# Performance work log

Hardware: AMD Instinct MI355X
Metric: run time of the kernel (lower is better)

## Reference

```python
import jax, jax.numpy as jnp
import numpy as np

B, S, H, NH, HD = 2, 2048, 4096, 32, 128
THETA = 10000.0


def rotate_half(x):
    x1, x2 = jnp.split(x, 2, axis=-1)
    return jnp.concatenate((-x2, x1), axis=-1)


def setup_inputs() -> dict:
    key = jax.random.key(0)
    ks = jax.random.split(key, 6)
    hidden_states = jax.random.normal(ks[0], (B, S, H), dtype=jnp.float32)
    # additive causal mask, [1,1,S,S]
    causal = jnp.triu(jnp.full((S, S), -1e9, dtype=jnp.float32), k=1)
    attention_mask = causal[None, None, :, :]
    scale = 0.02
    Wq = jax.random.normal(ks[1], (H, H), dtype=jnp.float32) * scale
    Wk = jax.random.normal(ks[2], (H, H), dtype=jnp.float32) * scale
    Wv = jax.random.normal(ks[3], (H, H), dtype=jnp.float32) * scale
    Wo = jax.random.normal(ks[4], (H, H), dtype=jnp.float32) * scale
    return {"hidden_states": hidden_states, "attention_mask": attention_mask,
            "Wq": Wq, "Wk": Wk, "Wv": Wv, "Wo": Wo}


def _rope_tables(seq_len, dtype):
    inv_freq = 1.0 / (THETA ** (jnp.arange(0, HD, 2, dtype=jnp.float32) / HD))
    t = jnp.arange(seq_len, dtype=jnp.float32)
    freqs = jnp.einsum('i,j->ij', t, inv_freq)          # [S, HD/2]
    emb = jnp.concatenate((freqs, freqs), axis=-1)       # [S, HD]
    return jnp.cos(emb).astype(dtype), jnp.sin(emb).astype(dtype)


def reference(hidden_states, attention_mask, Wq, Wk, Wv, Wo):
    b, s, _ = hidden_states.shape
    # nn.Linear: y = x @ W.T
    q = jnp.einsum('bsh,oh->bso', hidden_states, Wq).reshape(b, s, NH, HD).transpose(0, 2, 1, 3)
    k = jnp.einsum('bsh,oh->bso', hidden_states, Wk).reshape(b, s, NH, HD).transpose(0, 2, 1, 3)
    v = jnp.einsum('bsh,oh->bso', hidden_states, Wv).reshape(b, s, NH, HD).transpose(0, 2, 1, 3)
    cos, sin = _rope_tables(s, q.dtype)                  # [S, HD] broadcast over b,h
    q = q * cos + rotate_half(q) * sin
    k = k * cos + rotate_half(k) * sin
    scores = jnp.einsum('bhqd,bhkd->bhqk', q, k) / jnp.sqrt(jnp.asarray(HD, q.dtype))
    scores = scores + attention_mask
    attn = jax.nn.softmax(scores.astype(jnp.float32), axis=-1).astype(q.dtype)
    out = jnp.einsum('bhqk,bhkd->bhqd', attn, v)
    out = out.transpose(0, 2, 1, 3).reshape(b, s, H)
    return jnp.einsum('bsh,oh->bso', out, Wo)
```

## Files before the change

### kernel.cpp

```cpp
#include <hip/hip_runtime.h>
#include <stdint.h>

typedef __attribute__((ext_vector_type(4))) float f32x4;
typedef __attribute__((ext_vector_type(8))) short bf16x8;
typedef __attribute__((ext_vector_type(4))) unsigned int u32x4;

__device__ __forceinline__ short f2bf(float x) {
  unsigned int u = __builtin_bit_cast(unsigned int, x);
  unsigned int r = (u + 0x7fffu + ((u >> 16) & 1u)) >> 16;
  return (short)r;
}
__device__ __forceinline__ float bf2f(short s) {
  unsigned int u = ((unsigned int)(unsigned short)s) << 16;
  return __builtin_bit_cast(float, u);
}
__device__ __forceinline__ unsigned pkbf(float lo, float hi) {
  unsigned r;
  asm("v_cvt_pk_bf16_f32 %0, %1, %2" : "=v"(r) : "v"(lo), "v"(hi));
  return r;
}

__device__ __forceinline__ void gload_lds16(const void* g, void* l) {
  __builtin_amdgcn_global_load_lds(
      (const __attribute__((address_space(1))) void*)g,
      (__attribute__((address_space(3))) void*)l, 16, 0, 0);
}

__global__ __launch_bounds__(256) void cvt4(const float* __restrict__ a,
                                            const float* __restrict__ b,
                                            const float* __restrict__ c,
                                            const float* __restrict__ d,
                                            short* __restrict__ oa,
                                            short* __restrict__ ob,
                                            short* __restrict__ oc,
                                            short* __restrict__ od, int n) {
  const float* in = (blockIdx.y == 0) ? a : (blockIdx.y == 1) ? b : (blockIdx.y == 2) ? c : d;
  short* out = (blockIdx.y == 0) ? oa : (blockIdx.y == 1) ? ob : (blockIdx.y == 2) ? oc : od;
  int idx = blockIdx.x * blockDim.x + threadIdx.x;
  int stride = gridDim.x * blockDim.x;
  for (int i = idx * 4; i < n; i += stride * 4) {
    float4 v = *(const float4*)(in + i);
    short4 o;
    o.x = f2bf(v.x); o.y = f2bf(v.y); o.z = f2bf(v.z); o.w = f2bf(v.w);
    *(short4*)(out + i) = o;
  }
}

__global__ __launch_bounds__(256) void cvt_bf16(const float* __restrict__ in,
                                                short* __restrict__ out, int n) {
  int idx = blockIdx.x * blockDim.x + threadIdx.x;
  int stride = gridDim.x * blockDim.x;
  for (int i = idx * 4; i < n; i += stride * 4) {
    float4 v = *(const float4*)(in + i);
    short4 o;
    o.x = f2bf(v.x); o.y = f2bf(v.y); o.z = f2bf(v.z); o.w = f2bf(v.w);
    *(short4*)(out + i) = o;
  }
}

__global__ __launch_bounds__(256) void rope_table_k(float2* __restrict__ tab) {
  int idx = blockIdx.x * 256 + threadIdx.x;
  int s = idx >> 6, j = idx & 63;
  float invf = powf(10000.0f, -((float)j) / 64.0f);
  float a = (float)s * invf;
  tab[idx] = make_float2(cosf(a), sinf(a));
}

__global__ __launch_bounds__(256) void rope_apply_k(short* __restrict__ Qb,
                                                    short* __restrict__ Kb,
                                                    const float2* __restrict__ tab) {
  bool isK = (blockIdx.y != 0);
  short* base = isK ? Kb : Qb;
  float post = isK ? 1.0f : (0.08838834764831845f * 1.4426950408889634f);
  int token = blockIdx.x;
  int s = token & 2047;
  short* rowp = base + (size_t)token * 4096;
  const float2* trow = tab + s * 64;
  for (int u = threadIdx.x; u < 512; u += 256) {
    int h = u >> 4;
    int d0 = (u & 15) * 4;
    short* p1 = rowp + h * 128 + d0;
    short* p2 = p1 + 64;
    short4 a = *(short4*)p1, b = *(short4*)p2;
    short4 ra, rb;
#pragma unroll
    for (int j = 0; j < 4; ++j) {
      short aj = (&a.x)[j], bj = (&b.x)[j];
      float qa = bf2f(aj), qb = bf2f(bj);
      float2 cs = trow[d0 + j];
      (&ra.x)[j] = f2bf((qa * cs.x - qb * cs.y) * post);
      (&rb.x)[j] = f2bf((qb * cs.x + qa * cs.y) * post);
    }
    *(short4*)p1 = ra;
    *(short4*)p2 = rb;
  }
}

template <int MODE>
__global__ __launch_bounds__(512) void gemm256(const short* __restrict__ A,
                                               const short* __restrict__ Bw,
                                               void* __restrict__ out) {
  __shared__ __attribute__((aligned(16))) short smem[3 * 16384];
  int wg = blockIdx.x;
  int xcd = wg & 7, i = wg >> 3;
  int by = xcd * 2 + (i >> 4);
  int bx = i & 15;
  int tid = threadIdx.x;
  int w = tid >> 6, lane = tid & 63;
  int l16 = lane & 15, l4 = lane >> 4;
  int wm = w >> 2, wn = w & 3;

  f32x4 acc[8][4] = {};

  const short* Ab = A + (size_t)(by * 256) * 4096;
  const short* Bb = Bw + (size_t)(bx * 256) * 4096;
  int idx0 = tid, idx1 = 512 + tid;
  int r0 = idx0 >> 2, c0l = (idx0 & 3) ^ (r0 & 3);
  int r1 = idx1 >> 2, c1l = (idx1 & 3) ^ (r1 & 3);
  int db0 = (0 * 512 + w * 64) * 8;
  int db1 = (1 * 512 + w * 64) * 8;

  auto STAGE = [&](int kt, int ob) {
    gload_lds16(Ab + (size_t)r0 * 4096 + kt * 32 + c0l * 8, &smem[ob + db0]);
    gload_lds16(Ab + (size_t)r1 * 4096 + kt * 32 + c1l * 8, &smem[ob + db1]);
    gload_lds16(Bb + (size_t)r0 * 4096 + kt * 32 + c0l * 8, &smem[ob + 8192 + db0]);
    gload_lds16(Bb + (size_t)r1 * 4096 + kt * 32 + c1l * 8, &smem[ob + 8192 + db1]);
  };

  int o0 = 0, o1 = 16384, o2 = 32768;
  STAGE(0, o0);
  STAGE(1, o1);

  const int physc = l4 ^ (l16 & 3);
  const int arow = wm * 128 + l16;
  const int brow = wn * 64 + l16;

  auto COMPUTE = [&](int ob) {
    const short* lA = &smem[ob];
    const short* lB = &smem[ob + 8192];
    bf16x8 af[4], bfr[4];
#pragma unroll
    for (int nf = 0; nf < 4; ++nf)
      bfr[nf] = *(const bf16x8*)&lB[(brow + nf * 16) * 32 + physc * 8];
#pragma unroll
    for (int mf = 0; mf < 4; ++mf)
      af[mf] = *(const bf16x8*)&lA[(arow + mf * 16) * 32 + physc * 8];
    __builtin_amdgcn_s_setprio(1);
#pragma unroll
    for (int mf = 0; mf < 4; ++mf)
#pragma unroll
      for (int nf = 0; nf < 4; ++nf)
        acc[mf][nf] = __builtin_amdgcn_mfma_f32_16x16x32_bf16(af[mf], bfr[nf], acc[mf][nf], 0, 0, 0);
    __builtin_amdgcn_s_setprio(0);
#pragma unroll
    for (int mf = 0; mf < 4; ++mf)
      af[mf] = *(const bf16x8*)&lA[(arow + 64 + mf * 16) * 32 + physc * 8];
    __builtin_amdgcn_s_setprio(1);
#pragma unroll
    for (int mf = 0; mf < 4; ++mf)
#pragma unroll
      for (int nf = 0; nf < 4; ++nf)
        acc[mf + 4][nf] = __builtin_amdgcn_mfma_f32_16x16x32_bf16(af[mf], bfr[nf], acc[mf + 4][nf], 0, 0, 0);
    __builtin_amdgcn_s_setprio(0);
  };

  for (int t = 0; t < 127; ++t) {
    asm volatile("s_waitcnt vmcnt(4)" ::: "memory");
    __builtin_amdgcn_s_barrier();
    asm volatile("" ::: "memory");
    if (t + 2 < 128) STAGE(t + 2, o2);
    COMPUTE(o0);
    int tmp = o0; o0 = o1; o1 = o2; o2 = tmp;
  }
  asm volatile("s_waitcnt vmcnt(0)" ::: "memory");
  __builtin_amdgcn_s_barrier();
  asm volatile("" ::: "memory");
  COMPUTE(o0);

  int orow0 = by * 256 + wm * 128;
  int ocol0 = bx * 256 + wn * 64;
#pragma unroll
  for (int mf = 0; mf < 8; ++mf)
#pragma unroll
    for (int nf = 0; nf < 4; ++nf)
#pragma unroll
      for (int ii = 0; ii < 4; ++ii) {
        int r = orow0 + mf * 16 + l4 * 4 + ii;
        int c = ocol0 + nf * 16 + l16;
        float v = acc[mf][nf][ii];
        if constexpr (MODE == 0) {
          ((short*)out)[(size_t)r * 4096 + c] = f2bf(v);
        } else if constexpr (MODE == 1) {
          ((float*)out)[(size_t)r * 4096 + c] = v;
        } else {
          int bb = r >> 11, ss = r & 2047;
          int h = c >> 7, d = c & 127;
          ((short*)out)[(((size_t)((bb * 32 + h) * 128 + d)) << 11) + ss] = f2bf(v);
        }
      }
}

__global__ __launch_bounds__(256, 3) void attn_k(const short* __restrict__ Qb,
                                                 const short* __restrict__ Kb,
                                                 const short* __restrict__ Vt,
                                                 short* __restrict__ AO) {
  __shared__ __attribute__((aligned(16))) short smem[2 * 8192];
  int p = blockIdx.x;
  int bh = p & 63;
  int qt = 15 - (p >> 6);
  int b = bh >> 5, h = bh & 31;
  int tid = threadIdx.x, w = tid >> 6, lane = tid & 63;
  int l16 = lane & 15, l4 = lane >> 4;

  const int nt = 2 * qt + 2;
  const int qbase = qt * 128 + w * 32;

  bf16x8 qf[2][4];
  {
    const short* Qg = Qb + (size_t)(b * 2048 + qbase + l16) * 4096 + h * 128 + l4 * 8;
#pragma unroll
    for (int mg = 0; mg < 2; ++mg)
#pragma unroll
      for (int kk = 0; kk < 4; ++kk)
        qf[mg][kk] = *(const bf16x8*)(Qg + (size_t)mg * 16 * 4096 + kk * 32);
  }

  f32x4 oacc[2][8] = {};
  float mrun[2] = {-1e30f, -1e30f}, lsum[2] = {0.f, 0.f};

  const short* Kbase = Kb + (size_t)(b * 2048) * 4096 + h * 128;
  const short* Vbase = Vt + (size_t)bh * 128 * 2048;

  const int srowK = l4, skbK = l16;

  auto STAGE = [&](int t, int sel) {
    short* lK = &smem[sel * 8192];
#pragma unroll
    for (int ii = 0; ii < 4; ++ii) {
      int s = w * 4 + ii;
      int rowK = s * 4 + srowK;
      int srcK = skbK ^ (rowK & 15);
      gload_lds16(Kbase + (size_t)(t * 64 + rowK) * 4096 + srcK * 8, &lK[s * 512]);
    }
  };

  STAGE(0, 0);
  __syncthreads();

  const int src0 = l16 | ((2 * (l4 & 1)) << 4);
  const int src1 = src0 | 16;
  const bool hiA = (l4 >> 1) != 0;

  for (int t = 0; t < nt; ++t) {
    int sel = t & 1;
    if (t + 1 < nt) STAGE(t + 1, sel ^ 1);
    const short* lK = &smem[sel * 8192];

    bool skip = (t * 64 > qbase + 31);
    if (!skip) {
      f32x4 sacc[2][4] = {};
#pragma unroll
      for (int kk = 0; kk < 4; ++kk) {
#pragma unroll
        for (int n4 = 0; n4 < 4; ++n4) {
          int row = n4 * 16 + l16;
          int phys = (kk * 4 + l4) ^ (row & 15);
          bf16x8 kf = *(const bf16x8*)&lK[row * 128 + phys * 8];
          sacc[0][n4] = __builtin_amdgcn_mfma_f32_16x16x32_bf16(kf, qf[0][kk], sacc[0][n4], 0, 0, 0);
          sacc[1][n4] = __builtin_amdgcn_mfma_f32_16x16x32_bf16(kf, qf[1][kk], sacc[1][n4], 0, 0, 0);
        }
      }

      if (t * 64 + 63 > qbase) {
#pragma unroll
        for (int mg = 0; mg < 2; ++mg) {
          int q = qbase + mg * 16 + l16;
#pragma unroll
          for (int n4 = 0; n4 < 4; ++n4)
#pragma unroll
            for (int i = 0; i < 4; ++i) {
              int kv = t * 64 + n4 * 16 + l4 * 4 + i;
              if (kv > q) sacc[mg][n4][i] = -1e30f;
            }
        }
      }

#pragma unroll
      for (int mg = 0; mg < 2; ++mg) {
        float v0 = fmaxf(fmaxf(sacc[mg][0][0], sacc[mg][0][1]), fmaxf(sacc[mg][0][2], sacc[mg][0][3]));
        float v1 = fmaxf(fmaxf(sacc[mg][1][0], sacc[mg][1][1]), fmaxf(sacc[mg][1][2], sacc[mg][1][3]));
        float v2 = fmaxf(fmaxf(sacc[mg][2][0], sacc[mg][2][1]), fmaxf(sacc[mg][2][2], sacc[mg][2][3]));
        float v3 = fmaxf(fmaxf(sacc[mg][3][0], sacc[mg][3][1]), fmaxf(sacc[mg][3][2], sacc[mg][3][3]));
        float vm = fmaxf(fmaxf(v0, v1), fmaxf(v2, v3));
        vm = fmaxf(vm, __shfl_xor(vm, 16));
        vm = fmaxf(vm, __shfl_xor(vm, 32));
        float mn = mrun[mg];
        if (!__all(vm - mn <= 8.0f)) {
          float mnew = fmaxf(mn, vm);
          float fsc = __builtin_amdgcn_exp2f(mn - mnew);
          mrun[mg] = mnew;
          lsum[mg] *= fsc;
#pragma unroll
          for (int dg = 0; dg < 8; ++dg) oacc[mg][dg] *= fsc;
          mn = mnew;
        }
        float psum = 0.f;
#pragma unroll
        for (int n4 = 0; n4 < 4; ++n4)
#pragma unroll
          for (int i = 0; i < 4; ++i) {
            float e = __builtin_amdgcn_exp2f(sacc[mg][n4][i] - mn);
            sacc[mg][n4][i] = e;
            psum += e;
          }
        psum += __shfl_xor(psum, 16);
        psum += __shfl_xor(psum, 32);
        lsum[mg] += psum;
      }

      bf16x8 pb[2][2];
#pragma unroll
      for (int mg = 0; mg < 2; ++mg)
#pragma unroll
        for (int c = 0; c < 2; ++c) {
          unsigned pk0h0 = pkbf(sacc[mg][2 * c][0], sacc[mg][2 * c][1]);
          unsigned pk0h1 = pkbf(sacc[mg][2 * c][2], sacc[mg][2 * c][3]);
          unsigned pk1h0 = pkbf(sacc[mg][2 * c + 1][0], sacc[mg][2 * c + 1][1]);
          unsigned pk1h1 = pkbf(sacc[mg][2 * c + 1][2], sacc[mg][2 * c + 1][3]);
          unsigned s00 = __shfl((int)pk0h0, src0), s10 = __shfl((int)pk1h0, src0);
          unsigned s01 = __shfl((int)pk0h1, src0), s11 = __shfl((int)pk1h1, src0);
          unsigned t00 = __shfl((int)pk0h0, src1), t10 = __shfl((int)pk1h0, src1);
          unsigned t01 = __shfl((int)pk0h1, src1), t11 = __shfl((int)pk1h1, src1);
          u32x4 uw;
          uw[0] = hiA ? s10 : s00;
          uw[1] = hiA ? s11 : s01;
          uw[2] = hiA ? t10 : t00;
          uw[3] = hiA ? t11 : t01;
          pb[mg][c] = __builtin_bit_cast(bf16x8, uw);
        }

#pragma unroll
      for (int c = 0; c < 2; ++c) {
        const short* Vg = Vbase + t * 64 + c * 32 + l4 * 8;
#pragma unroll
        for (int dg = 0; dg < 8; ++dg) {
          bf16x8 vf = *(const bf16x8*)(Vg + (size_t)(dg * 16 + l16) * 2048);
          oacc[0][dg] = __builtin_amdgcn_mfma_f32_16x16x32_bf16(vf, pb[0][c], oacc[0][dg], 0, 0, 0);
          oacc[1][dg] = __builtin_amdgcn_mfma_f32_16x16x32_bf16(vf, pb[1][c], oacc[1][dg], 0, 0, 0);
        }
      }
    }
    __syncthreads();
  }

  short* reg = &smem[w * 4096];
  float rls0 = 1.0f / lsum[0], rls1 = 1.0f / lsum[1];
#pragma unroll
  for (int mg = 0; mg < 2; ++mg) {
    float rls = mg ? rls1 : rls0;
    int qloc = mg * 16 + l16;
#pragma unroll
    for (int dg = 0; dg < 8; ++dg) {
      unsigned u0 = pkbf(oacc[mg][dg][0] * rls, oacc[mg][dg][1] * rls);
      unsigned u1 = pkbf(oacc[mg][dg][2] * rls, oacc[mg][dg][3] * rls);
      int c16 = dg * 2 + (l4 >> 1);
      int phys = c16 ^ (qloc & 7);
      int sidx = qloc * 128 + phys * 8 + (l4 & 1) * 4;
      *(uint2*)&reg[sidx] = make_uint2(u0, u1);
    }
  }
#pragma unroll
  for (int pass = 0; pass < 8; ++pass) {
    int qloc = pass * 4 + l4;
    int phys = l16 ^ (qloc & 7);
    bf16x8 v = *(const bf16x8*)&reg[qloc * 128 + phys * 8];
    int qg = qt * 128 + w * 32 + qloc;
    *(bf16x8*)(AO + (size_t)(b * 2048 + qg) * 4096 + h * 128 + l16 * 8) = v;
  }
}

extern "C" void kernel_launch(void* const* d_in, const int* in_sizes, int n_in,
                              void* d_out, int out_size, void* d_ws, size_t ws_size,
                              hipStream_t stream) {
  const float* X = (const float*)d_in[0];
  const float* Wq = (const float*)d_in[2];
  const float* Wk = (const float*)d_in[3];
  const float* Wv = (const float*)d_in[4];
  const float* Wo = (const float*)d_in[5];

  char* ws = (char*)d_ws;
  const size_t SEG = 32ull << 20;
  short* Xb  = (short*)(ws + 0 * SEG);
  short* Wqb = (short*)(ws + 1 * SEG);
  short* Wkb = (short*)(ws + 2 * SEG);
  short* Wvb = (short*)(ws + 3 * SEG);
  short* Qb  = (short*)(ws + 4 * SEG);
  short* Kb  = (short*)(ws + 5 * SEG);
  float2* tab = (float2*)(ws + 6 * SEG);

  const int NE = 4096 * 4096;
  cvt4<<<dim3(2048, 4), 256, 0, stream>>>(X, Wq, Wk, Wv, Xb, Wqb, Wkb, Wvb, NE);
  rope_table_k<<<512, 256, 0, stream>>>(tab);

  gemm256<0><<<256, 512, 0, stream>>>(Xb, Wqb, Qb);
  gemm256<0><<<256, 512, 0, stream>>>(Xb, Wkb, Kb);
  short* Vtb = Wqb;
  gemm256<2><<<256, 512, 0, stream>>>(Xb, Wvb, Vtb);

  rope_apply_k<<<dim3(4096, 2), 256, 0, stream>>>(Qb, Kb, tab);

  short* AO = Xb;
  attn_k<<<1024, 256, 0, stream>>>(Qb, Kb, Vtb, AO);

  short* Wob = Wkb;
  cvt_bf16<<<2048, 256, 0, stream>>>(Wo, Wob, NE);
  gemm256<1><<<256, 512, 0, stream>>>(AO, Wob, (float*)d_out);
}
```

Measured before the change: 843.1 us.

## Stage V tiles through swizzled LDS and deepen K prefetch to two tiles

The attention kernel now loads V tiles asynchronously into a swizzled LDS buffer instead of reading them directly from global memory for each MFMA. K prefetch is deepened to two tiles ahead, with manual vmcnt waits and split barriers so V for the next tile loads while the current tile's QK and softmax run. This targets global-load latency on the PV matmul. In exchange, LDS use grows from 32 KB to 48 KB per block, which may cut occupancy, and the tile loop now carries extra barriers and hand-counted waits.

```diff
diff --git a/kernel.cpp b/kernel.cpp
--- a/kernel.cpp
+++ b/kernel.cpp
@@ -204,7 +204,7 @@
                                                  const short* __restrict__ Kb,
                                                  const short* __restrict__ Vt,
                                                  short* __restrict__ AO) {
-  __shared__ __attribute__((aligned(16))) short smem[2 * 8192];
+  __shared__ __attribute__((aligned(16))) short smem[24576];
   int p = blockIdx.x;
   int bh = p & 63;
   int qt = 15 - (p >> 6);
@@ -232,8 +232,9 @@
   const short* Vbase = Vt + (size_t)bh * 128 * 2048;
 
   const int srowK = l4, skbK = l16;
-
-  auto STAGE = [&](int t, int sel) {
+  const int srowV = lane >> 3, skbV = lane & 7;
+
+  auto STAGE_K = [&](int t, int sel) {
     short* lK = &smem[sel * 8192];
 #pragma unroll
     for (int ii = 0; ii < 4; ++ii) {
@@ -243,22 +244,35 @@
       gload_lds16(Kbase + (size_t)(t * 64 + rowK) * 4096 + srcK * 8, &lK[s * 512]);
     }
   };
-
-  STAGE(0, 0);
-  __syncthreads();
+  auto STAGE_V = [&](int t) {
+    short* lV = &smem[16384];
+#pragma unroll
+    for (int ii = 0; ii < 4; ++ii) {
+      int s = w * 4 + ii;
+      int rowV = s * 8 + srowV;
+      int srcV = skbV ^ (rowV & 7);
+      gload_lds16(Vbase + (size_t)rowV * 2048 + t * 64 + srcV * 8, &lV[s * 512]);
+    }
+  };
+
+  STAGE_V(0);
+  STAGE_K(0, 0);
+  STAGE_K(1, 1);
+  asm volatile("s_waitcnt vmcnt(4)" ::: "memory");
+  __builtin_amdgcn_s_barrier();
+  asm volatile("" ::: "memory");
 
   const int src0 = l16 | ((2 * (l4 & 1)) << 4);
   const int src1 = src0 | 16;
   const bool hiA = (l4 >> 1) != 0;
 
   for (int t = 0; t < nt; ++t) {
-    int sel = t & 1;
-    if (t + 1 < nt) STAGE(t + 1, sel ^ 1);
-    const short* lK = &smem[sel * 8192];
-
+    const short* lK = &smem[(t & 1) * 8192];
+    const short* lV = &smem[16384];
     bool skip = (t * 64 > qbase + 31);
+
+    f32x4 sacc[2][4] = {};
     if (!skip) {
-      f32x4 sacc[2][4] = {};
 #pragma unroll
       for (int kk = 0; kk < 4; ++kk) {
 #pragma unroll
@@ -317,7 +331,16 @@
         psum += __shfl_xor(psum, 32);
         lsum[mg] += psum;
       }
-
+    }
+
+    if (t == nt - 1)
+      asm volatile("s_waitcnt vmcnt(0)" ::: "memory");
+    else
+      asm volatile("s_waitcnt vmcnt(4)" ::: "memory");
+    __builtin_amdgcn_s_barrier();
+    asm volatile("" ::: "memory");
+
+    if (!skip) {
       bf16x8 pb[2][2];
 #pragma unroll
       for (int mg = 0; mg < 2; ++mg)
@@ -340,17 +363,27 @@
         }
 
 #pragma unroll
-      for (int c = 0; c < 2; ++c) {
-        const short* Vg = Vbase + t * 64 + c * 32 + l4 * 8;
+      for (int c = 0; c < 2; ++c)
 #pragma unroll
         for (int dg = 0; dg < 8; ++dg) {
-          bf16x8 vf = *(const bf16x8*)(Vg + (size_t)(dg * 16 + l16) * 2048);
+          int d = dg * 16 + l16;
+          int phys = (c * 4 + l4) ^ (d & 7);
+          bf16x8 vf = *(const bf16x8*)&lV[d * 64 + phys * 8];
           oacc[0][dg] = __builtin_amdgcn_mfma_f32_16x16x32_bf16(vf, pb[0][c], oacc[0][dg], 0, 0, 0);
           oacc[1][dg] = __builtin_amdgcn_mfma_f32_16x16x32_bf16(vf, pb[1][c], oacc[1][dg], 0, 0, 0);
         }
-      }
-    }
-    __syncthreads();
+    }
+
+    __builtin_amdgcn_s_barrier();
+    asm volatile("" ::: "memory");
+    if (t + 1 < nt) STAGE_V(t + 1);
+    if (t + 2 < nt) STAGE_K(t + 2, t & 1);
+    if (t + 2 < nt)
+      asm volatile("s_waitcnt vmcnt(8)" ::: "memory");
+    else if (t + 1 < nt)
+      asm volatile("s_waitcnt vmcnt(4)" ::: "memory");
+    __builtin_amdgcn_s_barrier();
+    asm volatile("" ::: "memory");
   }
 
   short* reg = &smem[w * 4096];
```

After: 761.6 us. -9.7%, faster.

## Restructure GEMM into 8-phase double-buffered K=64 pipeline and stage V via LDS

Applied to the files above, without the earlier changes.

The GEMM moves from a 3-stage K=32 ring buffer to a double-buffered K=64 tile with eight compute phases per two tiles. A and B loads are interleaved between phases, with a barrier after each phase, so global-to-LDS traffic overlaps MFMA work. Separately, the attention kernel now stages V tiles into LDS with an XOR swizzle alongside K, instead of reading V straight from global memory per MFMA. This doubles attention LDS use and drops the occupancy hint of 3, which may lower occupancy. The many per-phase barriers add synchronisation overhead.

```diff
diff --git a/kernel.cpp b/kernel.cpp
--- a/kernel.cpp
+++ b/kernel.cpp
@@ -97,14 +97,14 @@
 }
 
 template <int MODE>
-__global__ __launch_bounds__(512) void gemm256(const short* __restrict__ A,
-                                               const short* __restrict__ Bw,
-                                               void* __restrict__ out) {
-  __shared__ __attribute__((aligned(16))) short smem[3 * 16384];
+__global__ __launch_bounds__(512) void gemm8p(const short* __restrict__ A,
+                                              const short* __restrict__ Bw,
+                                              void* __restrict__ out) {
+  __shared__ __attribute__((aligned(16))) short smem[2 * 32768];
   int wg = blockIdx.x;
-  int xcd = wg & 7, i = wg >> 3;
-  int by = xcd * 2 + (i >> 4);
-  int bx = i & 15;
+  int xcd = wg & 7, ii = wg >> 3;
+  int by = xcd * 2 + (ii >> 4);
+  int bx = ii & 15;
   int tid = threadIdx.x;
   int w = tid >> 6, lane = tid & 63;
   int l16 = lane & 15, l4 = lane >> 4;
@@ -114,68 +114,83 @@
 
   const short* Ab = A + (size_t)(by * 256) * 4096;
   const short* Bb = Bw + (size_t)(bx * 256) * 4096;
-  int idx0 = tid, idx1 = 512 + tid;
-  int r0 = idx0 >> 2, c0l = (idx0 & 3) ^ (r0 & 3);
-  int r1 = idx1 >> 2, c1l = (idx1 & 3) ^ (r1 & 3);
-  int db0 = (0 * 512 + w * 64) * 8;
-  int db1 = (1 * 512 + w * 64) * 8;
-
-  auto STAGE = [&](int kt, int ob) {
-    gload_lds16(Ab + (size_t)r0 * 4096 + kt * 32 + c0l * 8, &smem[ob + db0]);
-    gload_lds16(Ab + (size_t)r1 * 4096 + kt * 32 + c1l * 8, &smem[ob + db1]);
-    gload_lds16(Bb + (size_t)r0 * 4096 + kt * 32 + c0l * 8, &smem[ob + 8192 + db0]);
-    gload_lds16(Bb + (size_t)r1 * 4096 + kt * 32 + c1l * 8, &smem[ob + 8192 + db1]);
+
+  auto STAGE_MAT = [&](int kt, int isB) {
+    const short* src = isB ? Bb : Ab;
+    int ob = (kt & 1) * 32768 + isB * 16384;
+#pragma unroll
+    for (int j = 0; j < 4; ++j) {
+      int c = j * 512 + tid;
+      int row = c >> 3;
+      int sc = (c & 7) ^ (row & 7);
+      gload_lds16(src + (size_t)row * 4096 + kt * 64 + sc * 8, &smem[ob + c * 8]);
+    }
   };
 
-  int o0 = 0, o1 = 16384, o2 = 32768;
-  STAGE(0, o0);
-  STAGE(1, o1);
-
-  const int physc = l4 ^ (l16 & 3);
-  const int arow = wm * 128 + l16;
-  const int brow = wn * 64 + l16;
-
-  auto COMPUTE = [&](int ob) {
+  bf16x8 bfr[4];
+  auto PHASE = [&](int ob, int kk, int mh, bool loadB) {
     const short* lA = &smem[ob];
-    const short* lB = &smem[ob + 8192];
-    bf16x8 af[4], bfr[4];
-#pragma unroll
-    for (int nf = 0; nf < 4; ++nf)
-      bfr[nf] = *(const bf16x8*)&lB[(brow + nf * 16) * 32 + physc * 8];
+    const short* lB = &smem[ob + 16384];
+    if (loadB) {
+#pragma unroll
+      for (int nf = 0; nf < 4; ++nf) {
+        int row = wn * 64 + nf * 16 + l16;
+        int phys = (kk * 4 + l4) ^ (row & 7);
+        bfr[nf] = *(const bf16x8*)&lB[row * 64 + phys * 8];
+      }
+    }
+    bf16x8 af[4];
+#pragma unroll
+    for (int mf = 0; mf < 4; ++mf) {
+      int row = wm * 128 + mh * 64 + mf * 16 + l16;
+      int phys = (kk * 4 + l4) ^ (row & 7);
+      af[mf] = *(const bf16x8*)&lA[row * 64 + phys * 8];
+    }
+    __builtin_amdgcn_s_setprio(1);
 #pragma unroll
     for (int mf = 0; mf < 4; ++mf)
-      af[mf] = *(const bf16x8*)&lA[(arow + mf * 16) * 32 + physc * 8];
-    __builtin_amdgcn_s_setprio(1);
-#pragma unroll
-    for (int mf = 0; mf < 4; ++mf)
 #pragma unroll
       for (int nf = 0; nf < 4; ++nf)
-        acc[mf][nf] = __builtin_amdgcn_mfma_f32_16x16x32_bf16(af[mf], bfr[nf], acc[mf][nf], 0, 0, 0);
+        acc[mh * 4 + mf][nf] =
+            __builtin_amdgcn_mfma_f32_16x16x32_bf16(af[mf], bfr[nf], acc[mh * 4 + mf][nf], 0, 0, 0);
     __builtin_amdgcn_s_setprio(0);
-#pragma unroll
-    for (int mf = 0; mf < 4; ++mf)
-      af[mf] = *(const bf16x8*)&lA[(arow + 64 + mf * 16) * 32 + physc * 8];
-    __builtin_amdgcn_s_setprio(1);
-#pragma unroll
-    for (int mf = 0; mf < 4; ++mf)
-#pragma unroll
-      for (int nf = 0; nf < 4; ++nf)
-        acc[mf + 4][nf] = __builtin_amdgcn_mfma_f32_16x16x32_bf16(af[mf], bfr[nf], acc[mf + 4][nf], 0, 0, 0);
-    __builtin_amdgcn_s_setprio(0);
+    __builtin_amdgcn_s_barrier();
+    asm volatile("" ::: "memory");
   };
 
-  for (int t = 0; t < 127; ++t) {
+  STAGE_MAT(0, 0);
+  STAGE_MAT(0, 1);
+  asm volatile("s_waitcnt vmcnt(0)" ::: "memory");
+  __builtin_amdgcn_s_barrier();
+  asm volatile("" ::: "memory");
+
+  const int b0 = 0, b1 = 32768;
+  for (int i = 0; i < 32; ++i) {
+    int kt1 = 2 * i + 1;
+
+    STAGE_MAT(kt1, 0);
     asm volatile("s_waitcnt vmcnt(4)" ::: "memory");
     __builtin_amdgcn_s_barrier();
     asm volatile("" ::: "memory");
-    if (t + 2 < 128) STAGE(t + 2, o2);
-    COMPUTE(o0);
-    int tmp = o0; o0 = o1; o1 = o2; o2 = tmp;
-  }
-  asm volatile("s_waitcnt vmcnt(0)" ::: "memory");
-  __builtin_amdgcn_s_barrier();
-  asm volatile("" ::: "memory");
-  COMPUTE(o0);
+    PHASE(b0, 0, 0, true);
+    STAGE_MAT(kt1, 1);
+    PHASE(b0, 0, 1, false);
+    PHASE(b0, 1, 0, true);
+    PHASE(b0, 1, 1, false);
+    if (i + 1 < 32) {
+      STAGE_MAT(2 * i + 2, 0);
+      asm volatile("s_waitcnt vmcnt(4)" ::: "memory");
+    } else {
+      asm volatile("s_waitcnt vmcnt(0)" ::: "memory");
+    }
+    __builtin_amdgcn_s_barrier();
+    asm volatile("" ::: "memory");
+    PHASE(b1, 0, 0, true);
+    if (i + 1 < 32) STAGE_MAT(2 * i + 2, 1);
+    PHASE(b1, 0, 1, false);
+    PHASE(b1, 1, 0, true);
+    PHASE(b1, 1, 1, false);
+  }
 
   int orow0 = by * 256 + wm * 128;
   int ocol0 = bx * 256 + wn * 64;
@@ -184,10 +199,10 @@
 #pragma unroll
     for (int nf = 0; nf < 4; ++nf)
 #pragma unroll
-      for (int ii = 0; ii < 4; ++ii) {
-        int r = orow0 + mf * 16 + l4 * 4 + ii;
+      for (int k = 0; k < 4; ++k) {
+        int r = orow0 + mf * 16 + l4 * 4 + k;
         int c = ocol0 + nf * 16 + l16;
-        float v = acc[mf][nf][ii];
+        float v = acc[mf][nf][k];
         if constexpr (MODE == 0) {
           ((short*)out)[(size_t)r * 4096 + c] = f2bf(v);
         } else if constexpr (MODE == 1) {
@@ -200,11 +215,11 @@
       }
 }
 
-__global__ __launch_bounds__(256, 3) void attn_k(const short* __restrict__ Qb,
-                                                 const short* __restrict__ Kb,
-                                                 const short* __restrict__ Vt,
-                                                 short* __restrict__ AO) {
-  __shared__ __attribute__((aligned(16))) short smem[2 * 8192];
+__global__ __launch_bounds__(256) void attn_k(const short* __restrict__ Qb,
+                                              const short* __restrict__ Kb,
+                                              const short* __restrict__ Vt,
+                                              short* __restrict__ AO) {
+  __shared__ __attribute__((aligned(16))) short smem[2 * 16384];
   int p = blockIdx.x;
   int bh = p & 63;
   int qt = 15 - (p >> 6);
@@ -232,15 +247,20 @@
   const short* Vbase = Vt + (size_t)bh * 128 * 2048;
 
   const int srowK = l4, skbK = l16;
+  const int srowV = lane >> 3, skbV = lane & 7;
 
   auto STAGE = [&](int t, int sel) {
-    short* lK = &smem[sel * 8192];
+    short* lK = &smem[sel * 16384];
+    short* lV = lK + 8192;
 #pragma unroll
     for (int ii = 0; ii < 4; ++ii) {
       int s = w * 4 + ii;
       int rowK = s * 4 + srowK;
       int srcK = skbK ^ (rowK & 15);
       gload_lds16(Kbase + (size_t)(t * 64 + rowK) * 4096 + srcK * 8, &lK[s * 512]);
+      int rowV = s * 8 + srowV;
+      int srcV = skbV ^ (rowV & 7);
+      gload_lds16(Vbase + (size_t)rowV * 2048 + t * 64 + srcV * 8, &lV[s * 512]);
     }
   };
 
@@ -254,7 +274,8 @@
   for (int t = 0; t < nt; ++t) {
     int sel = t & 1;
     if (t + 1 < nt) STAGE(t + 1, sel ^ 1);
-    const short* lK = &smem[sel * 8192];
+    const short* lK = &smem[sel * 16384];
+    const short* lV = lK + 8192;
 
     bool skip = (t * 64 > qbase + 31);
     if (!skip) {
@@ -340,15 +361,15 @@
         }
 
 #pragma unroll
-      for (int c = 0; c < 2; ++c) {
-        const short* Vg = Vbase + t * 64 + c * 32 + l4 * 8;
+      for (int c = 0; c < 2; ++c)
 #pragma unroll
         for (int dg = 0; dg < 8; ++dg) {
-          bf16x8 vf = *(const bf16x8*)(Vg + (size_t)(dg * 16 + l16) * 2048);
+          int d = dg * 16 + l16;
+          int phys = (c * 4 + l4) ^ (d & 7);
+          bf16x8 vf = *(const bf16x8*)&lV[d * 64 + phys * 8];
           oacc[0][dg] = __builtin_amdgcn_mfma_f32_16x16x32_bf16(vf, pb[0][c], oacc[0][dg], 0, 0, 0);
           oacc[1][dg] = __builtin_amdgcn_mfma_f32_16x16x32_bf16(vf, pb[1][c], oacc[1][dg], 0, 0, 0);
         }
-      }
     }
     __syncthreads();
   }
@@ -402,10 +423,10 @@
   cvt4<<<dim3(2048, 4), 256, 0, stream>>>(X, Wq, Wk, Wv, Xb, Wqb, Wkb, Wvb, NE);
   rope_table_k<<<512, 256, 0, stream>>>(tab);
 
-  gemm256<0><<<256, 512, 0, stream>>>(Xb, Wqb, Qb);
-  gemm256<0><<<256, 512, 0, stream>>>(Xb, Wkb, Kb);
+  gemm8p<0><<<256, 512, 0, stream>>>(Xb, Wqb, Qb);
+  gemm8p<0><<<256, 512, 0, stream>>>(Xb, Wkb, Kb);
   short* Vtb = Wqb;
-  gemm256<2><<<256, 512, 0, stream>>>(Xb, Wvb, Vtb);
+  gemm8p<2><<<256, 512, 0, stream>>>(Xb, Wvb, Vtb);
 
   rope_apply_k<<<dim3(4096, 2), 256, 0, stream>>>(Qb, Kb, tab);
 
@@ -414,5 +435,5 @@
 
   short* Wob = Wkb;
   cvt_bf16<<<2048, 256, 0, stream>>>(Wo, Wob, NE);
-  gemm256<1><<<256, 512, 0, stream>>>(AO, Wob, (float*)d_out);
-}
+  gemm8p<1><<<256, 512, 0, stream>>>(AO, Wob, (float*)d_out);
+}
```

After: 711.6 us. 1.18x faster.
